# Kernel tuning notes

Measured on AMD Instinct MI355X. Metric: run time of the kernel, lower is better.

The kernel has to match this reference:

```python
import jax, jax.numpy as jnp
import numpy as np

L, I, H = 4, 256, 512          # layers, input_size, hidden_size
SH, LH, GH = 4, 2, 2            # short/long/global heads
NH, HD, FF = SH + LH + GH, H // (SH + LH + GH), 2 * H
S, B = 1024, 8                  # seq (AST nodes), batch
EPS = 1e-5
NEG = -1e9


def _ln(x, g, b):
    m = jnp.mean(x, axis=-1, keepdims=True)
    v = jnp.var(x, axis=-1, keepdims=True)
    return (x - m) * jax.lax.rsqrt(v + EPS) * g + b


def setup_inputs() -> dict:
    key = jax.random.key(0)
    ks = jax.random.split(key, 10)
    w = lambda k, shape: jax.random.normal(k, shape, jnp.float32) * 0.02
    return {
        "nodes": jax.random.normal(ks[0], (S, B, I), jnp.float32),
        "dist": jax.random.randint(ks[1], (B, S, S), 0, 5, jnp.int32),
        "dense_w": w(ks[2], (H, I)), "dense_b": jnp.zeros((H,), jnp.float32),
        "dense_ln_g": jnp.ones((H,), jnp.float32), "dense_ln_b": jnp.zeros((H,), jnp.float32),
        "qkv_w": w(ks[3], (L, 3 * H, H)), "qkv_b": jnp.zeros((L, 3 * H), jnp.float32),
        "out_w": w(ks[4], (L, H, H)), "out_b": jnp.zeros((L, H), jnp.float32),
        "ln1_g": jnp.ones((L, H), jnp.float32), "ln1_b": jnp.zeros((L, H), jnp.float32),
        "ffn_w1": w(ks[5], (L, FF, H)), "ffn_b1": jnp.zeros((L, FF), jnp.float32),
        "ffn_w2": w(ks[6], (L, H, FF)), "ffn_b2": jnp.zeros((L, H), jnp.float32),
        "ln2_g": jnp.ones((L, H), jnp.float32), "ln2_b": jnp.zeros((L, H), jnp.float32),
        "bn_g": jnp.ones((H,), jnp.float32), "bn_b": jnp.zeros((H,), jnp.float32),
    }


def _mask_bias(dist):
    # dist: [B,S,S] int -> additive bias [B,NH,S,S]
    short = (dist == 1)[:, None]                       # [B,1,S,S]
    longm = (dist >= 1)[:, None]
    globm = jnp.broadcast_to((dist[:, 0:1, :] >= 1)[:, None], (dist.shape[0], 1, S, S))
    allowed = jnp.concatenate([
        jnp.broadcast_to(short, (dist.shape[0], SH, S, S)),
        jnp.broadcast_to(longm, (dist.shape[0], LH, S, S)),
        jnp.broadcast_to(globm, (dist.shape[0], GH, S, S)),
    ], axis=1)
    allowed = allowed | jnp.eye(S, dtype=bool)
    return jnp.where(allowed, 0.0, NEG).astype(jnp.float32)


def _forward(nodes, dist, dense_w, dense_b, dense_ln_g, dense_ln_b,
             qkv_w, qkv_b, out_w, out_b, ln1_g, ln1_b,
             ffn_w1, ffn_b1, ffn_w2, ffn_b2, ln2_g, ln2_b, bn_g, bn_b):
    x = jnp.transpose(nodes, (1, 0, 2))                # [B,S,I]
    x = _ln(x @ dense_w.T + dense_b, dense_ln_g, dense_ln_b)  # [B,S,H]
    bias = _mask_bias(dist)                            # [B,NH,S,S]
    scale = 1.0 / np.sqrt(HD)

    def layer(x, p):
        (wqkv, bqkv, wo, bo, g1, b1, w1, bf1, w2, bf2, g2, b2) = p
        qkv = x @ wqkv.T + bqkv                        # [B,S,3H]
        q, k, v = jnp.split(qkv, 3, axis=-1)
        q = q.reshape(B, S, NH, HD).transpose(0, 2, 1, 3)
        k = k.reshape(B, S, NH, HD).transpose(0, 2, 1, 3)
        v = v.reshape(B, S, NH, HD).transpose(0, 2, 1, 3)
        scores = jnp.einsum('bhqd,bhkd->bhqk', q, k) * scale + bias
        attn = jax.nn.softmax(scores, axis=-1)
        o = jnp.einsum('bhqk,bhkd->bhqd', attn, v)
        o = o.transpose(0, 2, 1, 3).reshape(B, S, H) @ wo.T + bo
        x = _ln(x + o, g1, b1)
        f = jax.nn.relu(x @ w1.T + bf1) @ w2.T + bf2
        x = _ln(x + f, g2, b2)
        return x, None

    params = (qkv_w, qkv_b, out_w, out_b, ln1_g, ln1_b,
              ffn_w1, ffn_b1, ffn_w2, ffn_b2, ln2_g, ln2_b)
    x, _ = jax.lax.scan(layer, x, params)
    hidden = x[:, 0]                                   # first token -> [B,H]
    m = jnp.mean(hidden, axis=0)
    v = jnp.var(hidden, axis=0)
    return (hidden - m) * jax.lax.rsqrt(v + EPS) * bn_g + bn_b


def reference(nodes, dist, dense_w, dense_b, dense_ln_g, dense_ln_b,
              qkv_w, qkv_b, out_w, out_b, ln1_g, ln1_b,
              ffn_w1, ffn_b1, ffn_w2, ffn_b2, ln2_g, ln2_b, bn_g, bn_b):
    return _forward(nodes, dist, dense_w, dense_b, dense_ln_g, dense_ln_b,
                    qkv_w, qkv_b, out_w, out_b, ln1_g, ln1_b,
                    ffn_w1, ffn_b1, ffn_w2, ffn_b2, ln2_g, ln2_b, bn_g, bn_b)
```

## Files before the change

kernel.cpp:

```cpp
#include <hip/hip_runtime.h>
#include <hip/hip_bf16.h>
#include <math.h>

#define LAYERS 4
#define IDIM 256
#define HDIM 512
#define NH 8
#define HD 64
#define FF 1024
#define SEQ 1024
#define BATCH 8
#define EPS 1e-5f

typedef __attribute__((ext_vector_type(8))) short short8;
typedef __attribute__((ext_vector_type(4))) short short4v;
typedef __attribute__((ext_vector_type(4))) float f32x4;
typedef __attribute__((ext_vector_type(4))) int int4v;
typedef __attribute__((ext_vector_type(4))) unsigned int uint4v;
typedef unsigned long long u64;

__device__ __forceinline__ short f2bf(float f) {
    unsigned u = __float_as_uint(f);
    u = (u + 0x7FFFu + ((u >> 16) & 1u)) >> 16;
    return (short)u;
}
__device__ __forceinline__ float bf2f(short s) {
    return __uint_as_float(((unsigned)(unsigned short)s) << 16);
}
__device__ __forceinline__ void gll16(const void* g, void* l) {
    __builtin_amdgcn_global_load_lds(
        (const __attribute__((address_space(1))) unsigned int*)g,
        (__attribute__((address_space(3))) unsigned int*)l, 16, 0, 0);
}
__device__ __forceinline__ float fexp2(float x) {
#if __has_builtin(__builtin_amdgcn_exp2f)
    return __builtin_amdgcn_exp2f(x);
#else
    return exp2f(x);
#endif
}

#define BAR() __builtin_amdgcn_s_barrier()
#define SCHED0() __builtin_amdgcn_sched_barrier(0)
#define VM4() asm volatile("s_waitcnt vmcnt(4)" ::: "memory")
#define VM2() asm volatile("s_waitcnt vmcnt(2)" ::: "memory")
#define VM0() asm volatile("s_waitcnt vmcnt(0)" ::: "memory")
#define LGKM0() asm volatile("s_waitcnt lgkmcnt(0)" ::: "memory")

#define CVT_P0 131072u
#define CVT_P1 3276800u
#define CVT_P2 4325376u
#define CVT_P3 6422528u
#define CVT_TOT 8519680u
#define PREP_W 8320
#define PREP_N 2048
__global__ __launch_bounds__(256) void prep_all(
    const float* __restrict__ s0, short* __restrict__ d0,
    const float* __restrict__ s1, short* __restrict__ d1,
    const float* __restrict__ s2, short* __restrict__ d2,
    const float* __restrict__ s3, short* __restrict__ d3,
    const float* __restrict__ s4, short* __restrict__ d4,
    const float* __restrict__ nodes, short* __restrict__ xt,
    const int* __restrict__ dist, u64* __restrict__ mS,
    u64* __restrict__ mL, u64* __restrict__ mG) {
    int blk = blockIdx.x;
    if (blk < PREP_W) {
        size_t i = ((size_t)blk * 256 + threadIdx.x) * 4;
        const float* s; short* d; size_t off;
        if (i < CVT_P0)      { s = s0; d = d0; off = i; }
        else if (i < CVT_P1) { s = s1; d = d1; off = i - CVT_P0; }
        else if (i < CVT_P2) { s = s2; d = d2; off = i - CVT_P1; }
        else if (i < CVT_P3) { s = s3; d = d3; off = i - CVT_P2; }
        else                 { s = s4; d = d4; off = i - CVT_P3; }
        f32x4 f = *(const f32x4*)(s + off);
        short4v o = {f2bf(f[0]), f2bf(f[1]), f2bf(f[2]), f2bf(f[3])};
        *(short4v*)(d + off) = o;
    } else if (blk < PREP_W + PREP_N) {
        size_t idx = ((size_t)(blk - PREP_W) * 256 + threadIdx.x) * 4;
        int i  = idx & (IDIM - 1);
        int sb = idx >> 8;
        int b  = sb & (BATCH - 1);
        int s  = sb >> 3;
        f32x4 f = *(const f32x4*)(nodes + idx);
        short4v o = {f2bf(f[0]), f2bf(f[1]), f2bf(f[2]), f2bf(f[3])};
        *(short4v*)(xt + ((size_t)b * SEQ + s) * IDIM + i) = o;
    } else {
        int blk2 = blk - (PREP_W + PREP_N);
        int b = blk2 >> 10, q = blk2 & 1023;
        int wv = threadIdx.x >> 6, lane = threadIdx.x & 63;
        const int* dp = dist + ((size_t)b * SEQ + q) * SEQ;
        size_t mbase = ((size_t)b * SEQ + q) * 16;
#pragma unroll
        for (int it = 0; it < 4; it++) {
            int w64 = it * 4 + wv;
            int d = dp[w64 * 64 + lane];
            u64 bs = __ballot(d == 1);
            u64 bl = __ballot(d >= 1);
            if (lane == 0) {
                mS[mbase + w64] = bs;
                mL[mbase + w64] = bl;
                if (q == 0) mG[b * 16 + w64] = bl;
            }
        }
    }
}

template<int BM, int BK>
__global__ __launch_bounds__(256, 2)
void gemm_bf16(const short* __restrict__ A, const short* __restrict__ W,
               const float* __restrict__ bias, short* __restrict__ C,
               short* __restrict__ vt, int M, int N, int K, int relu) {
    constexpr int UPR = BK / 8;
    constexpr int RPC = 512 / BK;
    __shared__ __align__(16) short As[BM * BK];
    __shared__ __align__(16) short Ws[128 * BK];
    const int tid = threadIdx.x;
    const int w = tid >> 6, lane = tid & 63;
    const int l15 = lane & 15, quad = lane >> 4;
    const int m0 = blockIdx.y * BM, n0 = blockIdx.x * 128;

    constexpr int NI = (BM == 128) ? 4 : 2;
    const int wm = (BM == 128) ? (w >> 1) * 64 : 0;
    const int wn = (BM == 128) ? (w & 1) * 64 : w * 32;

    f32x4 acc[4][NI];
#pragma unroll
    for (int mi = 0; mi < 4; mi++)
#pragma unroll
        for (int ni = 0; ni < NI; ni++) acc[mi][ni] = (f32x4){0.f, 0.f, 0.f, 0.f};

    const int r_in = (BK == 64) ? (lane >> 3) : (lane >> 4);
    const int c8   = lane & (UPR - 1);

    for (int k0 = 0; k0 < K; k0 += BK) {
#pragma unroll
        for (int rep = 0; rep < BM * BK / 2048; rep++) {
            int chunk = rep * 4 + w;
            int row = chunk * RPC + r_in;
            const short* src = A + (size_t)(m0 + row) * K + k0 + ((c8 ^ (row & (UPR - 1))) << 3);
            gll16(src, (char*)As + chunk * 1024);
        }
#pragma unroll
        for (int rep = 0; rep < 128 * BK / 2048; rep++) {
            int chunk = rep * 4 + w;
            int row = chunk * RPC + r_in;
            const short* src = W + (size_t)(n0 + row) * K + k0 + ((c8 ^ (row & (UPR - 1))) << 3);
            gll16(src, (char*)Ws + chunk * 1024);
        }
        __syncthreads();
#pragma unroll
        for (int ks = 0; ks < BK / 32; ks++) {
            short8 af[4], wf[NI];
            const int dblk = ks * 4 + quad;
#pragma unroll
            for (int mi = 0; mi < 4; mi++) {
                int row = wm + mi * 16 + l15;
                af[mi] = *(const short8*)((const char*)As + row * (BK * 2) + ((dblk ^ (row & (UPR - 1))) << 4));
            }
#pragma unroll
            for (int ni = 0; ni < NI; ni++) {
                int row = wn + ni * 16 + l15;
                wf[ni] = *(const short8*)((const char*)Ws + row * (BK * 2) + ((dblk ^ (row & (UPR - 1))) << 4));
            }
#pragma unroll
            for (int mi = 0; mi < 4; mi++)
#pragma unroll
                for (int ni = 0; ni < NI; ni++)
                    acc[mi][ni] = __builtin_amdgcn_mfma_f32_16x16x32_bf16(
                        af[mi], wf[ni], acc[mi][ni], 0, 0, 0);
        }
        __syncthreads();
    }
    if (vt && n0 >= 1024) {
#pragma unroll
        for (int ni = 0; ni < NI; ni++) {
            int n = n0 + wn + ni * 16 + l15;
            int d = n - 1024, h = d >> 6, dd = d & 63;
            float bz = bias[n];
#pragma unroll
            for (int mi = 0; mi < 4; mi++) {
                int mbase = m0 + wm + mi * 16 + quad * 4;
                int b = mbase >> 10, s = mbase & 1023;
                size_t off = ((size_t)(b * NH + h) * HD + dd) * SEQ + s;
                short4v pk;
#pragma unroll
                for (int r = 0; r < 4; r++) pk[r] = f2bf(acc[mi][ni][r] + bz);
                *(short4v*)(vt + off) = pk;
            }
        }
    } else {
#pragma unroll
        for (int ni = 0; ni < NI; ni++) {
            int n = n0 + wn + ni * 16 + l15;
            float bz = bias[n];
#pragma unroll
            for (int mi = 0; mi < 4; mi++) {
#pragma unroll
                for (int r = 0; r < 4; r++) {
                    int m = m0 + wm + mi * 16 + quad * 4 + r;
                    float v = acc[mi][ni][r] + bz;
                    if (relu) v = fmaxf(v, 0.f);
                    C[(size_t)m * N + n] = f2bf(v);
                }
            }
        }
    }
}

template<int K, bool RES>
__global__ __launch_bounds__(512, 1)
void gemm_ln(const short* __restrict__ A, const short* __restrict__ W,
             const float* __restrict__ bias, const short* __restrict__ resid,
             const float* __restrict__ g, const float* __restrict__ bta,
             short* __restrict__ Y) {
    constexpr int NT = K / 16;
    constexpr int KCN = K / 32;
    __shared__ __align__(16) char smem[81920];
    char* Apan = smem;
    char* Wb   = smem + 32768;
    float* red = (float*)smem;

    const int tid = threadIdx.x, w = tid >> 6, lane = tid & 63;
    const int l15 = lane & 15, quad = lane >> 4;
    const int m0 = blockIdx.x * 32;
    const int r4 = lane >> 2, c4 = lane & 3;

    f32x4 acc[2][4];
#pragma unroll
    for (int mi = 0; mi < 2; mi++)
#pragma unroll
        for (int j = 0; j < 4; j++) acc[mi][j] = (f32x4){0.f, 0.f, 0.f, 0.f};

    if constexpr (K == 512) {
#pragma unroll
        for (int j = 0; j < 4; j++) {
            int row = j * 8 + w;
            gll16(A + (size_t)(m0 + row) * K + ((lane ^ (row & 7)) << 3),
                  Apan + row * 1024);
        }
    } else {
#pragma unroll
        for (int j = 0; j < 2; j++) {
            int li = j * 8 + w;
            int row = li * 2 + (lane >> 5);
            gll16(A + (size_t)(m0 + row) * K + (((lane & 31) ^ (row & 7)) << 3),
                  Apan + li * 1024);
        }
    }
#define GLN_ISSUE(c, bp_)                                                     \
    do {                                                                      \
        int rg_ = (c) & 1, kc_ = (c) >> 1;                                    \
        _Pragma("unroll")                                                     \
        for (int j_ = 0; j_ < 2; j_++) {                                      \
            int li_ = j_ * 8 + w;                                             \
            int gr_ = rg_ * 256 + li_ * 16 + r4;                              \
            gll16(W + (size_t)gr_ * K + kc_ * 32 + ((c4 ^ (r4 & 3)) << 3),    \
                  (bp_) + li_ * 1024);                                        \
        }                                                                     \
    } while (0)
    GLN_ISSUE(0, Wb);
    GLN_ISSUE(1, Wb + 16384);
    GLN_ISSUE(2, Wb + 32768);
    VM4();
    BAR(); SCHED0();

    int cur = 0;
    for (int kc = 0; kc < KCN; kc++) {
        short8 af[2];
#pragma unroll
        for (int mi = 0; mi < 2; mi++) {
            int ar = mi * 16 + l15;
            af[mi] = *(const short8*)(Apan + ar * (K * 2) +
                                      (((kc * 4 + quad) ^ (ar & 7)) << 4));
        }
#pragma unroll
        for (int rg = 0; rg < 2; rg++) {
            const char* bp = Wb + cur * 16384;
#pragma unroll
            for (int ni = 0; ni < 2; ni++) {
                int rr = w * 32 + ni * 16 + l15;
                short8 wf = *(const short8*)(bp + rr * 64 + ((quad ^ (rr & 3)) << 4));
#pragma unroll
                for (int mi = 0; mi < 2; mi++)
                    acc[mi][rg * 2 + ni] = __builtin_amdgcn_mfma_f32_16x16x32_bf16(
                        wf, af[mi], acc[mi][rg * 2 + ni], 0, 0, 0);
            }
            BAR(); SCHED0();
            {
                int c = kc * 2 + rg + 3;
                if (c < NT)           { GLN_ISSUE(c, Wb + cur * 16384); VM4(); }
                else if (c == NT)     VM2();
                else if (c == NT + 1) VM0();
            }
            BAR(); SCHED0();
            cur = (cur == 2) ? 0 : cur + 1;
        }
    }
#undef GLN_ISSUE

    float sum[2] = {0.f, 0.f}, sq[2] = {0.f, 0.f};
#pragma unroll
    for (int mi = 0; mi < 2; mi++)
#pragma unroll
        for (int j = 0; j < 4; j++) {
            int nb = (j >> 1) * 256 + w * 32 + (j & 1) * 16 + quad * 4;
            f32x4 bz = *(const f32x4*)(bias + nb);
            f32x4 v;
            if (RES) {
                short4v rv = *(const short4v*)(resid + (size_t)(m0 + mi * 16 + l15) * HDIM + nb);
#pragma unroll
                for (int r = 0; r < 4; r++) v[r] = acc[mi][j][r] + bz[r] + bf2f(rv[r]);
            } else {
#pragma unroll
                for (int r = 0; r < 4; r++) v[r] = acc[mi][j][r] + bz[r];
            }
            acc[mi][j] = v;
            sum[mi] += v[0] + v[1] + v[2] + v[3];
            sq[mi]  += v[0] * v[0] + v[1] * v[1] + v[2] * v[2] + v[3] * v[3];
        }
#pragma unroll
    for (int mi = 0; mi < 2; mi++) {
        sum[mi] += __shfl_xor(sum[mi], 16); sum[mi] += __shfl_xor(sum[mi], 32);
        sq[mi]  += __shfl_xor(sq[mi], 16);  sq[mi]  += __shfl_xor(sq[mi], 32);
    }
    if (quad == 0) {
#pragma unroll
        for (int mi = 0; mi < 2; mi++) {
            red[(mi * 16 + l15) * 8 + w]       = sum[mi];
            red[256 + (mi * 16 + l15) * 8 + w] = sq[mi];
        }
    }
    __syncthreads();
    float mean[2], inv[2];
#pragma unroll
    for (int mi = 0; mi < 2; mi++) {
        f32x4 s0 = *(const f32x4*)(red + (mi * 16 + l15) * 8);
        f32x4 s1 = *(const f32x4*)(red + (mi * 16 + l15) * 8 + 4);
        f32x4 q0 = *(const f32x4*)(red + 256 + (mi * 16 + l15) * 8);
        f32x4 q1 = *(const f32x4*)(red + 256 + (mi * 16 + l15) * 8 + 4);
        float st = s0[0] + s0[1] + s0[2] + s0[3] + s1[0] + s1[1] + s1[2] + s1[3];
        float qt = q0[0] + q0[1] + q0[2] + q0[3] + q1[0] + q1[1] + q1[2] + q1[3];
        float mn = st * (1.f / HDIM);
        float vr = qt * (1.f / HDIM) - mn * mn;
        mean[mi] = mn;
        inv[mi]  = rsqrtf(vr + EPS);
    }
#pragma unroll
    for (int mi = 0; mi < 2; mi++)
#pragma unroll
        for (int j = 0; j < 4; j++) {
            int nb = (j >> 1) * 256 + w * 32 + (j & 1) * 16 + quad * 4;
            f32x4 gv = *(const f32x4*)(g + nb);
            f32x4 bv = *(const f32x4*)(bta + nb);
            short4v pk;
#pragma unroll
            for (int r = 0; r < 4; r++)
                pk[r] = f2bf((acc[mi][j][r] - mean[mi]) * inv[mi] * gv[r] + bv[r]);
            *(short4v*)(Y + (size_t)(m0 + mi * 16 + l15) * HDIM + nb) = pk;
        }
}

__global__ __launch_bounds__(512, 1)
void fused_ffn(const short* __restrict__ X, const short* __restrict__ W1,
               const float* __restrict__ b1, const short* __restrict__ W2,
               const float* __restrict__ b2, const float* __restrict__ g,
               const float* __restrict__ bta, short* __restrict__ Y) {
    __shared__ __align__(16) char smem[147456];
    char* Apan = smem;
    char* Wb   = smem + 32768;
    char* Hs   = smem + 81920;
    float* red = (float*)smem;

    const int tid = threadIdx.x, w = tid >> 6, lane = tid & 63;
    const int l15 = lane & 15, quad = lane >> 4;
    const int m0 = blockIdx.x * 32;
    const int r4 = lane >> 2, c4 = lane & 3;

    f32x4 acc1[2][8];
#pragma unroll
    for (int mi = 0; mi < 2; mi++)
#pragma unroll
        for (int j = 0; j < 8; j++) acc1[mi][j] = (f32x4){0.f, 0.f, 0.f, 0.f};

#pragma unroll
    for (int j = 0; j < 4; j++) {
        int row = j * 8 + w;
        gll16(X + (size_t)(m0 + row) * HDIM + ((lane ^ (row & 7)) << 3),
              Apan + row * 1024);
    }
#define FF1_ISSUE(c, bp_)                                                     \
    do {                                                                      \
        int rg_ = (c) & 3, kc_ = (c) >> 2;                                    \
        _Pragma("unroll")                                                     \
        for (int j_ = 0; j_ < 2; j_++) {                                      \
            int li_ = j_ * 8 + w;                                             \
            int gr_ = rg_ * 256 + li_ * 16 + r4;                              \
            gll16(W1 + (size_t)gr_ * HDIM + kc_ * 32 + ((c4 ^ (r4 & 3)) << 3),\
                  (bp_) + li_ * 1024);                                        \
        }                                                                     \
    } while (0)
#define FF2_ISSUE(c, bp_)                                                     \
    do {                                                                      \
        int rg_ = (c) & 1, kc_ = (c) >> 1;                                    \
        _Pragma("unroll")                                                     \
        for (int j_ = 0; j_ < 2; j_++) {                                      \
            int li_ = j_ * 8 + w;                                             \
            int gr_ = rg_ * 256 + li_ * 16 + r4;                              \
            gll16(W2 + (size_t)gr_ * FF + kc_ * 32 + ((c4 ^ (r4 & 3)) << 3),  \
                  (bp_) + li_ * 1024);                                        \
        }                                                                     \
    } while (0)
    FF1_ISSUE(0, Wb);
    FF1_ISSUE(1, Wb + 16384);
    FF1_ISSUE(2, Wb + 32768);
    VM4();
    BAR(); SCHED0();

    int cur = 0;
    for (int kc = 0; kc < 16; kc++) {
        short8 af[2];
#pragma unroll
        for (int mi = 0; mi < 2; mi++) {
            int ar = mi * 16 + l15;
            af[mi] = *(const short8*)(Apan + ar * 1024 +
                                      (((kc * 4 + quad) ^ (ar & 7)) << 4));
        }
#pragma unroll
        for (int rg = 0; rg < 4; rg++) {
            const char* bp = Wb + cur * 16384;
#pragma unroll
            for (int ni = 0; ni < 2; ni++) {
                int rr = w * 32 + ni * 16 + l15;
                short8 wf = *(const short8*)(bp + rr * 64 + ((quad ^ (rr & 3)) << 4));
#pragma unroll
                for (int mi = 0; mi < 2; mi++)
                    acc1[mi][rg * 2 + ni] = __builtin_amdgcn_mfma_f32_16x16x32_bf16(
                        wf, af[mi], acc1[mi][rg * 2 + ni], 0, 0, 0);
            }
            BAR(); SCHED0();
            {
                int c = kc * 4 + rg + 3;
                if (c < 64)      { FF1_ISSUE(c, Wb + cur * 16384); VM4(); }
                else if (c == 64) VM2();
                else if (c == 65) VM0();
            }
            BAR(); SCHED0();
            cur = (cur == 2) ? 0 : cur + 1;
        }
    }

    FF2_ISSUE(0, Wb);
    FF2_ISSUE(1, Wb + 16384);
    FF2_ISSUE(2, Wb + 32768);
#pragma unroll
    for (int mi = 0; mi < 2; mi++)
#pragma unroll
        for (int j = 0; j < 8; j++) {
            int n = (j >> 1) * 256 + w * 32 + (j & 1) * 16 + quad * 4;
            f32x4 bz = *(const f32x4*)(b1 + n);
            short4v pk;
#pragma unroll
            for (int r = 0; r < 4; r++)
                pk[r] = f2bf(fmaxf(acc1[mi][j][r] + bz[r], 0.f));
            int row = mi * 16 + l15;
            int u = n >> 3;
            *(short4v*)(Hs + row * 2048 + ((u ^ (row & 7)) << 4) + (quad & 1) * 8) = pk;
        }
    LGKM0();
    VM4();
    BAR(); SCHED0();

    f32x4 acc2[2][4];
#pragma unroll
    for (int mi = 0; mi < 2; mi++)
#pragma unroll
        for (int j = 0; j < 4; j++) acc2[mi][j] = (f32x4){0.f, 0.f, 0.f, 0.f};

    cur = 0;
    for (int kc = 0; kc < 32; kc++) {
        short8 af[2];
#pragma unroll
        for (int mi = 0; mi < 2; mi++) {
            int ar = mi * 16 + l15;
            af[mi] = *(const short8*)(Hs + ar * 2048 +
                                      (((kc * 4 + quad) ^ (ar & 7)) << 4));
        }
#pragma unroll
        for (int rg = 0; rg < 2; rg++) {
            const char* bp = Wb + cur * 16384;
#pragma unroll
            for (int ni = 0; ni < 2; ni++) {
                int rr = w * 32 + ni * 16 + l15;
                short8 wf = *(const short8*)(bp + rr * 64 + ((quad ^ (rr & 3)) << 4));
#pragma unroll
                for (int mi = 0; mi < 2; mi++)
                    acc2[mi][rg * 2 + ni] = __builtin_amdgcn_mfma_f32_16x16x32_bf16(
                        wf, af[mi], acc2[mi][rg * 2 + ni], 0, 0, 0);
            }
            BAR(); SCHED0();
            {
                int c = kc * 2 + rg + 3;
                if (c < 64)      { FF2_ISSUE(c, Wb + cur * 16384); VM4(); }
                else if (c == 64) VM2();
                else if (c == 65) VM0();
            }
            BAR(); SCHED0();
            cur = (cur == 2) ? 0 : cur + 1;
        }
    }
#undef FF1_ISSUE
#undef FF2_ISSUE

    float sum[2] = {0.f, 0.f}, sq[2] = {0.f, 0.f};
#pragma unroll
    for (int mi = 0; mi < 2; mi++)
#pragma unroll
        for (int j = 0; j < 4; j++) {
            int nb = (j >> 1) * 256 + w * 32 + (j & 1) * 16 + quad * 4;
            f32x4 bz = *(const f32x4*)(b2 + nb);
            short4v rv = *(const short4v*)(X + (size_t)(m0 + mi * 16 + l15) * HDIM + nb);
            f32x4 v;
#pragma unroll
            for (int r = 0; r < 4; r++) v[r] = acc2[mi][j][r] + bz[r] + bf2f(rv[r]);
            acc2[mi][j] = v;
            sum[mi] += v[0] + v[1] + v[2] + v[3];
            sq[mi]  += v[0] * v[0] + v[1] * v[1] + v[2] * v[2] + v[3] * v[3];
        }
#pragma unroll
    for (int mi = 0; mi < 2; mi++) {
        sum[mi] += __shfl_xor(sum[mi], 16); sum[mi] += __shfl_xor(sum[mi], 32);
        sq[mi]  += __shfl_xor(sq[mi], 16);  sq[mi]  += __shfl_xor(sq[mi], 32);
    }
    if (quad == 0) {
#pragma unroll
        for (int mi = 0; mi < 2; mi++) {
            red[(mi * 16 + l15) * 8 + w]       = sum[mi];
            red[256 + (mi * 16 + l15) * 8 + w] = sq[mi];
        }
    }
    __syncthreads();
    float mean[2], inv[2];
#pragma unroll
    for (int mi = 0; mi < 2; mi++) {
        f32x4 s0 = *(const f32x4*)(red + (mi * 16 + l15) * 8);
        f32x4 s1 = *(const f32x4*)(red + (mi * 16 + l15) * 8 + 4);
        f32x4 q0 = *(const f32x4*)(red + 256 + (mi * 16 + l15) * 8);
        f32x4 q1 = *(const f32x4*)(red + 256 + (mi * 16 + l15) * 8 + 4);
        float st = s0[0] + s0[1] + s0[2] + s0[3] + s1[0] + s1[1] + s1[2] + s1[3];
        float qt = q0[0] + q0[1] + q0[2] + q0[3] + q1[0] + q1[1] + q1[2] + q1[3];
        float mn = st * (1.f / HDIM);
        float vr = qt * (1.f / HDIM) - mn * mn;
        mean[mi] = mn;
        inv[mi]  = rsqrtf(vr + EPS);
    }
#pragma unroll
    for (int mi = 0; mi < 2; mi++)
#pragma unroll
        for (int j = 0; j < 4; j++) {
            int nb = (j >> 1) * 256 + w * 32 + (j & 1) * 16 + quad * 4;
            f32x4 gv = *(const f32x4*)(g + nb);
            f32x4 bv = *(const f32x4*)(bta + nb);
            short4v pk;
#pragma unroll
            for (int r = 0; r < 4; r++)
                pk[r] = f2bf((acc2[mi][j][r] - mean[mi]) * inv[mi] * gv[r] + bv[r]);
            *(short4v*)(Y + (size_t)(m0 + mi * 16 + l15) * HDIM + nb) = pk;
        }
}

#define EXP2SC 0.18033688011112042f
__global__ __launch_bounds__(256, 4)
void attn_mfma(const short* __restrict__ qkv, const short* __restrict__ vt,
               const u64* __restrict__ maskS, const u64* __restrict__ maskL,
               const u64* __restrict__ maskG, short* __restrict__ out) {
    const int tid = threadIdx.x;
    const int w = tid >> 6, lane = tid & 63, l15 = lane & 15, quad = lane >> 4;
    const int p = blockIdx.x;
    const int g_ = (p & 7) + 8 * (p >> 7);
    const int qt = (p >> 3) & 15;
    const int b = g_ >> 3, h = g_ & 7;
    const int q = qt * 64 + w * 16 + l15;

    __shared__ __align__(16) short Ks[128 * 64];
    __shared__ __align__(16) short Vs[128 * 64];

    short8 qf[2];
    {
        const short* qrow = qkv + ((size_t)(b * SEQ + q) * 1536) + h * 64;
#pragma unroll
        for (int ks = 0; ks < 2; ks++)
            qf[ks] = *(const short8*)(qrow + ks * 32 + quad * 8);
    }
    const u64* mrow = (h < 4) ? (maskS + ((size_t)b * SEQ + q) * 16)
                   : (h < 6) ? (maskL + ((size_t)b * SEQ + q) * 16)
                   :           (maskG + (size_t)b * 16);

    f32x4 of[4];
#pragma unroll
    for (int mt = 0; mt < 4; mt++) of[mt] = (f32x4){0.f, 0.f, 0.f, 0.f};
    float ls0 = 0.f, ls1 = 0.f;

    const int r_in = lane >> 3, c8 = lane & 7;
    const int swz = (c8 ^ r_in) << 3;
    const short* kbase = qkv + ((size_t)b * SEQ) * 1536 + 512 + h * 64 + swz;
    const short* vp = vt + ((size_t)((b * NH + h) * HD) + r_in) * SEQ + swz;
    const int fsw = (l15 & 7);

    for (int kt = 0; kt < SEQ; kt += 128) {
#pragma unroll
        for (int rep = 0; rep < 4; rep++) {
            int c = rep * 4 + w;
            int pr = c * 8 + r_in;
            int pt = pr & 63;
            int key = (pr & 64) | (pt & 32) | (((pt >> 2) & 3) << 3)
                    | (((pt >> 4) & 1) << 2) | (pt & 3);
            gll16(kbase + (size_t)(kt + key) * 1536, (char*)Ks + c * 1024);
        }
#pragma unroll
        for (int rep = 0; rep < 4; rep++) {
            int v = rep * 4 + w;
            gll16(vp + (size_t)((v & 7) * 8) * SEQ + kt + (v >> 3) * 64,
                  (char*)Vs + v * 1024);
        }
        __syncthreads();

#pragma unroll
        for (int t = 0; t < 2; t++) {
            f32x4 sa[4];
#pragma unroll
            for (int g = 0; g < 4; g++) sa[g] = (f32x4){0.f, 0.f, 0.f, 0.f};
#pragma unroll
            for (int ks = 0; ks < 2; ks++) {
                const int dblk = ks * 4 + quad;
#pragma unroll
                for (int g = 0; g < 4; g++) {
                    int row = t * 64 + g * 16 + l15;
                    short8 kf = *(const short8*)((const char*)Ks + row * 128 + ((dblk ^ fsw) << 4));
                    sa[g] = __builtin_amdgcn_mfma_f32_16x16x32_bf16(kf, qf[ks], sa[g], 0, 0, 0);
                }
            }
            u64 mw = mrow[(kt >> 6) + t];
            if ((q >> 6) == (kt >> 6) + t) mw |= 1ull << (q & 63);
            u64 mq2 = mw >> (quad * 8);
            unsigned mlo = (unsigned)mq2, mhi = (unsigned)(mq2 >> 32);
            float pv[4][4];
#pragma unroll
            for (int g = 0; g < 4; g++) {
                unsigned mg = ((g & 2) ? mhi : mlo) >> ((g & 1) * 4);
#pragma unroll
                for (int r = 0; r < 4; r++) {
                    float e = fexp2(sa[g][r] * EXP2SC);
                    e = ((mg >> r) & 1u) ? e : 0.f;
                    pv[g][r] = e;
                    if (g & 1) ls1 += e; else ls0 += e;
                }
            }
            short8 pfrag[2];
#pragma unroll
            for (int g32 = 0; g32 < 2; g32++) {
                uint4v pk;
                pk[0] = __builtin_amdgcn_perm(__float_as_uint(pv[2 * g32][1]),
                                              __float_as_uint(pv[2 * g32][0]), 0x07060302u);
                pk[1] = __builtin_amdgcn_perm(__float_as_uint(pv[2 * g32][3]),
                                              __float_as_uint(pv[2 * g32][2]), 0x07060302u);
                pk[2] = __builtin_amdgcn_perm(__float_as_uint(pv[2 * g32 + 1][1]),
                                              __float_as_uint(pv[2 * g32 + 1][0]), 0x07060302u);
                pk[3] = __builtin_amdgcn_perm(__float_as_uint(pv[2 * g32 + 1][3]),
                                              __float_as_uint(pv[2 * g32 + 1][2]), 0x07060302u);
                pfrag[g32] = __builtin_bit_cast(short8, pk);
            }
#pragma unroll
            for (int g32 = 0; g32 < 2; g32++) {
                const int u = g32 * 4 + quad;
#pragma unroll
                for (int mt = 0; mt < 4; mt++) {
                    int row = mt * 16 + l15;
                    short8 vf = *(const short8*)((const char*)Vs + t * 8192 + row * 128 + ((u ^ fsw) << 4));
                    of[mt] = __builtin_amdgcn_mfma_f32_16x16x32_bf16(vf, pfrag[g32], of[mt], 0, 0, 0);
                }
            }
        }
        __syncthreads();
    }
    float lsum = ls0 + ls1;
    lsum += __shfl_xor(lsum, 16);
    lsum += __shfl_xor(lsum, 32);
    float inv = 1.f / lsum;
#pragma unroll
    for (int mt = 0; mt < 4; mt++) {
        short4v pk;
#pragma unroll
        for (int r = 0; r < 4; r++) pk[r] = f2bf(of[mt][r] * inv);
        *(short4v*)(out + ((size_t)(b * SEQ + q) * HDIM) + h * 64 + mt * 16 + quad * 4) = pk;
    }
}

__global__ __launch_bounds__(256) void final_bn(const short* __restrict__ X,
                                                const float* __restrict__ g,
                                                const float* __restrict__ bb,
                                                float* __restrict__ out) {
    int h = blockIdx.x * 256 + threadIdx.x;
    if (h >= HDIM) return;
    float vals[BATCH];
    float m = 0.f;
#pragma unroll
    for (int b = 0; b < BATCH; b++) {
        vals[b] = bf2f(X[(size_t)b * SEQ * HDIM + h]);
        m += vals[b];
    }
    m *= (1.f / BATCH);
    float v = 0.f;
#pragma unroll
    for (int b = 0; b < BATCH; b++) { float d = vals[b] - m; v += d * d; }
    v *= (1.f / BATCH);
    float inv = rsqrtf(v + EPS);
#pragma unroll
    for (int b = 0; b < BATCH; b++)
        out[b * HDIM + h] = (vals[b] - m) * inv * g[h] + bb[h];
}

extern "C" void kernel_launch(void* const* d_in, const int* in_sizes, int n_in,
                              void* d_out, int out_size, void* d_ws, size_t ws_size,
                              hipStream_t stream) {
    const float* nodes      = (const float*)d_in[0];
    const int*   dist       = (const int*)  d_in[1];
    const float* dense_w    = (const float*)d_in[2];
    const float* dense_b    = (const float*)d_in[3];
    const float* dense_ln_g = (const float*)d_in[4];
    const float* dense_ln_b = (const float*)d_in[5];
    const float* qkv_w      = (const float*)d_in[6];
    const float* qkv_b      = (const float*)d_in[7];
    const float* out_w      = (const float*)d_in[8];
    const float* out_b      = (const float*)d_in[9];
    const float* ln1_g      = (const float*)d_in[10];
    const float* ln1_b      = (const float*)d_in[11];
    const float* ffn_w1     = (const float*)d_in[12];
    const float* ffn_b1     = (const float*)d_in[13];
    const float* ffn_w2     = (const float*)d_in[14];
    const float* ffn_b2     = (const float*)d_in[15];
    const float* ln2_g      = (const float*)d_in[16];
    const float* ln2_b      = (const float*)d_in[17];
    const float* bn_g       = (const float*)d_in[18];
    const float* bn_b       = (const float*)d_in[19];
    float* out = (float*)d_out;

    const int M = BATCH * SEQ;
    const size_t MB = 1024 * 1024;
    char* ws = (char*)d_ws;
    short* Wd   = (short*)(ws + 0 * MB);
    short* Wqkv = (short*)(ws + 1 * MB);
    short* Wo   = (short*)(ws + 9 * MB);
    short* W1   = (short*)(ws + 13 * MB);
    short* W2   = (short*)(ws + 18 * MB);
    u64*   mS   = (u64*)(ws + 23 * MB);
    u64*   mL   = (u64*)(ws + 24 * MB);
    u64*   mG   = (u64*)(ws + 25 * MB);
    short* X    = (short*)(ws + 26 * MB);
    short* QKV  = (short*)(ws + 34 * MB);
    short* Vt   = (short*)(ws + 58 * MB);
    short* AT   = (short*)(ws + 66 * MB);
    short* XT   = QKV;

    prep_all<<<PREP_W + PREP_N + BATCH * SEQ, 256, 0, stream>>>(
        dense_w, Wd, qkv_w, Wqkv, out_w, Wo, ffn_w1, W1, ffn_w2, W2,
        nodes, XT, dist, mS, mL, mG);

    gemm_ln<IDIM, false><<<M / 32, 512, 0, stream>>>(
        XT, Wd, dense_b, nullptr, dense_ln_g, dense_ln_b, X);

    for (int l = 0; l < LAYERS; l++) {
        const short* wqkv = Wqkv + (size_t)l * 3 * HDIM * HDIM;
        const float* bqkv = qkv_b + (size_t)l * 3 * HDIM;
        const short* wo   = Wo + (size_t)l * HDIM * HDIM;
        const float* bo   = out_b + (size_t)l * HDIM;
        const short* w1   = W1 + (size_t)l * FF * HDIM;
        const float* b1   = ffn_b1 + (size_t)l * FF;
        const short* w2   = W2 + (size_t)l * HDIM * FF;
        const float* b2   = ffn_b2 + (size_t)l * HDIM;

        gemm_bf16<128, 64><<<dim3(3 * HDIM / 128, M / 128), 256, 0, stream>>>(
            X, wqkv, bqkv, QKV, Vt, M, 3 * HDIM, HDIM, 0);
        attn_mfma<<<1024, 256, 0, stream>>>(QKV, Vt, mS, mL, mG, AT);
        gemm_ln<HDIM, true><<<M / 32, 512, 0, stream>>>(
            AT, wo, bo, X, ln1_g + l * HDIM, ln1_b + l * HDIM, X);
        fused_ffn<<<M / 32, 512, 0, stream>>>(
            X, w1, b1, w2, b2, ln2_g + l * HDIM, ln2_b + l * HDIM, X);
    }
    final_bn<<<(HDIM + 255) / 256, 256, 0, stream>>>(X, bn_g, bn_b, out);
}
```

Measured before the change: 615.3 us.

## Widen weight K-stages to 64 and restructure LDS ring pipelining in gemm_ln and fused_ffn

```diff
diff --git a/kernel.cpp b/kernel.cpp
--- a/kernel.cpp
+++ b/kernel.cpp
@@ -43,7 +43,6 @@
 #define BAR() __builtin_amdgcn_s_barrier()
 #define SCHED0() __builtin_amdgcn_sched_barrier(0)
 #define VM4() asm volatile("s_waitcnt vmcnt(4)" ::: "memory")
-#define VM2() asm volatile("s_waitcnt vmcnt(2)" ::: "memory")
 #define VM0() asm volatile("s_waitcnt vmcnt(0)" ::: "memory")
 #define LGKM0() asm volatile("s_waitcnt lgkmcnt(0)" ::: "memory")
 
@@ -213,17 +212,17 @@
              const float* __restrict__ bias, const short* __restrict__ resid,
              const float* __restrict__ g, const float* __restrict__ bta,
              short* __restrict__ Y) {
-    constexpr int NT = K / 16;
-    constexpr int KCN = K / 32;
-    __shared__ __align__(16) char smem[81920];
+    constexpr int NCH = K / 32;
+    __shared__ __align__(16) char smem[K * 64 + 98304];
     char* Apan = smem;
-    char* Wb   = smem + 32768;
+    char* ring = smem + K * 64;
     float* red = (float*)smem;
 
     const int tid = threadIdx.x, w = tid >> 6, lane = tid & 63;
     const int l15 = lane & 15, quad = lane >> 4;
     const int m0 = blockIdx.x * 32;
-    const int r4 = lane >> 2, c4 = lane & 3;
+    const int rin8 = lane >> 3, c8 = lane & 7;
+    const int swz8 = (c8 ^ rin8) << 3;
 
     f32x4 acc[2][4];
 #pragma unroll
@@ -241,62 +240,62 @@
     } else {
 #pragma unroll
         for (int j = 0; j < 2; j++) {
-            int li = j * 8 + w;
-            int row = li * 2 + (lane >> 5);
+            int seg = j * 8 + w;
+            int row = seg * 2 + (lane >> 5);
             gll16(A + (size_t)(m0 + row) * K + (((lane & 31) ^ (row & 7)) << 3),
-                  Apan + li * 1024);
-        }
-    }
-#define GLN_ISSUE(c, bp_)                                                     \
+                  Apan + seg * 1024);
+        }
+    }
+#define GISS(c)                                                               \
     do {                                                                      \
-        int rg_ = (c) & 1, kc_ = (c) >> 1;                                    \
+        int rg_ = (c) & 1, kst_ = (c) >> 1;                                   \
+        char* bp_ = ring + ((c) % 3) * 32768;                                 \
         _Pragma("unroll")                                                     \
-        for (int j_ = 0; j_ < 2; j_++) {                                      \
-            int li_ = j_ * 8 + w;                                             \
-            int gr_ = rg_ * 256 + li_ * 16 + r4;                              \
-            gll16(W + (size_t)gr_ * K + kc_ * 32 + ((c4 ^ (r4 & 3)) << 3),    \
-                  (bp_) + li_ * 1024);                                        \
+        for (int j_ = 0; j_ < 4; j_++) {                                      \
+            int seg_ = j_ * 8 + w;                                            \
+            int ric_ = seg_ * 8 + rin8;                                       \
+            gll16(W + (size_t)(rg_ * 256 + ric_) * K + kst_ * 64 + swz8,      \
+                  bp_ + seg_ * 1024);                                         \
         }                                                                     \
     } while (0)
-    GLN_ISSUE(0, Wb);
-    GLN_ISSUE(1, Wb + 16384);
-    GLN_ISSUE(2, Wb + 32768);
+
+    GISS(0); GISS(1);
     VM4();
     BAR(); SCHED0();
 
-    int cur = 0;
-    for (int kc = 0; kc < KCN; kc++) {
-        short8 af[2];
-#pragma unroll
-        for (int mi = 0; mi < 2; mi++) {
-            int ar = mi * 16 + l15;
-            af[mi] = *(const short8*)(Apan + ar * (K * 2) +
-                                      (((kc * 4 + quad) ^ (ar & 7)) << 4));
-        }
-#pragma unroll
-        for (int rg = 0; rg < 2; rg++) {
-            const char* bp = Wb + cur * 16384;
-#pragma unroll
-            for (int ni = 0; ni < 2; ni++) {
-                int rr = w * 32 + ni * 16 + l15;
-                short8 wf = *(const short8*)(bp + rr * 64 + ((quad ^ (rr & 3)) << 4));
-#pragma unroll
-                for (int mi = 0; mi < 2; mi++)
-                    acc[mi][rg * 2 + ni] = __builtin_amdgcn_mfma_f32_16x16x32_bf16(
-                        wf, af[mi], acc[mi][rg * 2 + ni], 0, 0, 0);
-            }
+    for (int c = 0; c < NCH; c++) {
+        if (c + 2 < NCH) GISS(c + 2);
+        {
+            int kst = c >> 1, rg = c & 1;
+            const char* bp = ring + (c % 3) * 32768;
+#pragma unroll
+            for (int ks = 0; ks < 2; ks++) {
+                short8 af[2];
+#pragma unroll
+                for (int mi = 0; mi < 2; mi++) {
+                    int ar = mi * 16 + l15;
+                    af[mi] = *(const short8*)(Apan + ar * (K * 2) +
+                        (((kst * 8 + ks * 4 + quad) ^ (ar & 7)) << 4));
+                }
+#pragma unroll
+                for (int ni = 0; ni < 2; ni++) {
+                    int rr = w * 32 + ni * 16 + l15;
+                    short8 wf = *(const short8*)(bp + rr * 128 +
+                        (((ks * 4 + quad) ^ (rr & 7)) << 4));
+#pragma unroll
+                    for (int mi = 0; mi < 2; mi++)
+                        acc[mi][rg * 2 + ni] = __builtin_amdgcn_mfma_f32_16x16x32_bf16(
+                            wf, af[mi], acc[mi][rg * 2 + ni], 0, 0, 0);
+                }
+            }
+        }
+        if (c + 1 < NCH) {
+            if (c + 2 < NCH) VM4(); else VM0();
             BAR(); SCHED0();
-            {
-                int c = kc * 2 + rg + 3;
-                if (c < NT)           { GLN_ISSUE(c, Wb + cur * 16384); VM4(); }
-                else if (c == NT)     VM2();
-                else if (c == NT + 1) VM0();
-            }
-            BAR(); SCHED0();
-            cur = (cur == 2) ? 0 : cur + 1;
-        }
-    }
-#undef GLN_ISSUE
+        }
+    }
+#undef GISS
+    __syncthreads();
 
     float sum[2] = {0.f, 0.f}, sq[2] = {0.f, 0.f};
 #pragma unroll
@@ -365,16 +364,18 @@
                const float* __restrict__ b1, const short* __restrict__ W2,
                const float* __restrict__ b2, const float* __restrict__ g,
                const float* __restrict__ bta, short* __restrict__ Y) {
-    __shared__ __align__(16) char smem[147456];
+    __shared__ __align__(16) char smem[131072];
     char* Apan = smem;
-    char* Wb   = smem + 32768;
-    char* Hs   = smem + 81920;
-    float* red = (float*)smem;
+    char* ring = smem + 32768;
+    char* Hs   = smem;
+    char* W2b  = smem + 65536;
+    float* red = (float*)(smem + 65536);
 
     const int tid = threadIdx.x, w = tid >> 6, lane = tid & 63;
     const int l15 = lane & 15, quad = lane >> 4;
     const int m0 = blockIdx.x * 32;
-    const int r4 = lane >> 2, c4 = lane & 3;
+    const int rin8 = lane >> 3, c8 = lane & 7;
+    const int swz8 = (c8 ^ rin8) << 3;
 
     f32x4 acc1[2][8];
 #pragma unroll
@@ -388,70 +389,69 @@
         gll16(X + (size_t)(m0 + row) * HDIM + ((lane ^ (row & 7)) << 3),
               Apan + row * 1024);
     }
-#define FF1_ISSUE(c, bp_)                                                     \
+#define F1ISS(c)                                                              \
     do {                                                                      \
-        int rg_ = (c) & 3, kc_ = (c) >> 2;                                    \
+        int rg_ = (c) & 3, kst_ = (c) >> 2;                                   \
+        char* bp_ = ring + ((c) % 3) * 32768;                                 \
         _Pragma("unroll")                                                     \
-        for (int j_ = 0; j_ < 2; j_++) {                                      \
-            int li_ = j_ * 8 + w;                                             \
-            int gr_ = rg_ * 256 + li_ * 16 + r4;                              \
-            gll16(W1 + (size_t)gr_ * HDIM + kc_ * 32 + ((c4 ^ (r4 & 3)) << 3),\
-                  (bp_) + li_ * 1024);                                        \
+        for (int j_ = 0; j_ < 4; j_++) {                                      \
+            int seg_ = j_ * 8 + w;                                            \
+            int ric_ = seg_ * 8 + rin8;                                       \
+            gll16(W1 + (size_t)(rg_ * 256 + ric_) * HDIM + kst_ * 64 + swz8,  \
+                  bp_ + seg_ * 1024);                                         \
         }                                                                     \
     } while (0)
-#define FF2_ISSUE(c, bp_)                                                     \
+#define F2ISS(c)                                                              \
     do {                                                                      \
-        int rg_ = (c) & 1, kc_ = (c) >> 1;                                    \
+        int rg_ = (c) & 1, kst_ = (c) >> 1;                                   \
+        char* bp_ = W2b + ((c) & 1) * 32768;                                  \
         _Pragma("unroll")                                                     \
-        for (int j_ = 0; j_ < 2; j_++) {                                      \
-            int li_ = j_ * 8 + w;                                             \
-            int gr_ = rg_ * 256 + li_ * 16 + r4;                              \
-            gll16(W2 + (size_t)gr_ * FF + kc_ * 32 + ((c4 ^ (r4 & 3)) << 3),  \
-                  (bp_) + li_ * 1024);                                        \
+        for (int j_ = 0; j_ < 4; j_++) {                                      \
+            int seg_ = j_ * 8 + w;                                            \
+            int ric_ = seg_ * 8 + rin8;                                       \
+            gll16(W2 + (size_t)(rg_ * 256 + ric_) * FF + kst_ * 64 + swz8,    \
+                  bp_ + seg_ * 1024);                                         \
         }                                                                     \
     } while (0)
-    FF1_ISSUE(0, Wb);
-    FF1_ISSUE(1, Wb + 16384);
-    FF1_ISSUE(2, Wb + 32768);
+
+    F1ISS(0); F1ISS(1);
     VM4();
     BAR(); SCHED0();
 
-    int cur = 0;
-    for (int kc = 0; kc < 16; kc++) {
-        short8 af[2];
-#pragma unroll
-        for (int mi = 0; mi < 2; mi++) {
-            int ar = mi * 16 + l15;
-            af[mi] = *(const short8*)(Apan + ar * 1024 +
-                                      (((kc * 4 + quad) ^ (ar & 7)) << 4));
-        }
-#pragma unroll
-        for (int rg = 0; rg < 4; rg++) {
-            const char* bp = Wb + cur * 16384;
-#pragma unroll
-            for (int ni = 0; ni < 2; ni++) {
-                int rr = w * 32 + ni * 16 + l15;
-                short8 wf = *(const short8*)(bp + rr * 64 + ((quad ^ (rr & 3)) << 4));
-#pragma unroll
-                for (int mi = 0; mi < 2; mi++)
-                    acc1[mi][rg * 2 + ni] = __builtin_amdgcn_mfma_f32_16x16x32_bf16(
-                        wf, af[mi], acc1[mi][rg * 2 + ni], 0, 0, 0);
-            }
+    for (int c = 0; c < 32; c++) {
+        if (c + 2 < 32) F1ISS(c + 2);
+        {
+            int kst = c >> 2, rg = c & 3;
+            const char* bp = ring + (c % 3) * 32768;
+#pragma unroll
+            for (int ks = 0; ks < 2; ks++) {
+                short8 af[2];
+#pragma unroll
+                for (int mi = 0; mi < 2; mi++) {
+                    int ar = mi * 16 + l15;
+                    af[mi] = *(const short8*)(Apan + ar * 1024 +
+                        (((kst * 8 + ks * 4 + quad) ^ (ar & 7)) << 4));
+                }
+#pragma unroll
+                for (int ni = 0; ni < 2; ni++) {
+                    int rr = w * 32 + ni * 16 + l15;
+                    short8 wf = *(const short8*)(bp + rr * 128 +
+                        (((ks * 4 + quad) ^ (rr & 7)) << 4));
+#pragma unroll
+                    for (int mi = 0; mi < 2; mi++)
+                        acc1[mi][rg * 2 + ni] = __builtin_amdgcn_mfma_f32_16x16x32_bf16(
+                            wf, af[mi], acc1[mi][rg * 2 + ni], 0, 0, 0);
+                }
+            }
+        }
+        if (c + 1 < 32) {
+            if (c + 2 < 32) VM4(); else VM0();
             BAR(); SCHED0();
-            {
-                int c = kc * 4 + rg + 3;
-                if (c < 64)      { FF1_ISSUE(c, Wb + cur * 16384); VM4(); }
-                else if (c == 64) VM2();
-                else if (c == 65) VM0();
-            }
-            BAR(); SCHED0();
-            cur = (cur == 2) ? 0 : cur + 1;
-        }
-    }
-
-    FF2_ISSUE(0, Wb);
-    FF2_ISSUE(1, Wb + 16384);
-    FF2_ISSUE(2, Wb + 32768);
+        }
+    }
+    __syncthreads();
+
+    F2ISS(0); F2ISS(1);
 #pragma unroll
     for (int mi = 0; mi < 2; mi++)
 #pragma unroll
@@ -476,40 +476,39 @@
 #pragma unroll
         for (int j = 0; j < 4; j++) acc2[mi][j] = (f32x4){0.f, 0.f, 0.f, 0.f};
 
-    cur = 0;
-    for (int kc = 0; kc < 32; kc++) {
-        short8 af[2];
-#pragma unroll
-        for (int mi = 0; mi < 2; mi++) {
-            int ar = mi * 16 + l15;
-            af[mi] = *(const short8*)(Hs + ar * 2048 +
-                                      (((kc * 4 + quad) ^ (ar & 7)) << 4));
-        }
-#pragma unroll
-        for (int rg = 0; rg < 2; rg++) {
-            const char* bp = Wb + cur * 16384;
-#pragma unroll
-            for (int ni = 0; ni < 2; ni++) {
-                int rr = w * 32 + ni * 16 + l15;
-                short8 wf = *(const short8*)(bp + rr * 64 + ((quad ^ (rr & 3)) << 4));
-#pragma unroll
-                for (int mi = 0; mi < 2; mi++)
-                    acc2[mi][rg * 2 + ni] = __builtin_amdgcn_mfma_f32_16x16x32_bf16(
-                        wf, af[mi], acc2[mi][rg * 2 + ni], 0, 0, 0);
-            }
+    for (int c = 0; c < 32; c++) {
+        {
+            int kst = c >> 1, rg = c & 1;
+            const char* bp = W2b + (c & 1) * 32768;
+#pragma unroll
+            for (int ks = 0; ks < 2; ks++) {
+                short8 af[2];
+#pragma unroll
+                for (int mi = 0; mi < 2; mi++) {
+                    int ar = mi * 16 + l15;
+                    af[mi] = *(const short8*)(Hs + ar * 2048 +
+                        (((kst * 8 + ks * 4 + quad) ^ (ar & 7)) << 4));
+                }
+#pragma unroll
+                for (int ni = 0; ni < 2; ni++) {
+                    int rr = w * 32 + ni * 16 + l15;
+                    short8 wf = *(const short8*)(bp + rr * 128 +
+                        (((ks * 4 + quad) ^ (rr & 7)) << 4));
+#pragma unroll
+                    for (int mi = 0; mi < 2; mi++)
+                        acc2[mi][rg * 2 + ni] = __builtin_amdgcn_mfma_f32_16x16x32_bf16(
+                            wf, af[mi], acc2[mi][rg * 2 + ni], 0, 0, 0);
+                }
+            }
+        }
+        if (c + 1 < 32) {
             BAR(); SCHED0();
-            {
-                int c = kc * 2 + rg + 3;
-                if (c < 64)      { FF2_ISSUE(c, Wb + cur * 16384); VM4(); }
-                else if (c == 64) VM2();
-                else if (c == 65) VM0();
-            }
+            if (c + 2 < 32) { F2ISS(c + 2); VM4(); } else VM0();
             BAR(); SCHED0();
-            cur = (cur == 2) ? 0 : cur + 1;
-        }
-    }
-#undef FF1_ISSUE
-#undef FF2_ISSUE
+        }
+    }
+#undef F1ISS
+#undef F2ISS
 
     float sum[2] = {0.f, 0.f}, sq[2] = {0.f, 0.f};
 #pragma unroll
```

Result: faster. 573.6 us (-6.8%).
